# Optimization experiments

Measured on AMD Instinct MI355X. Metric: run time of the kernel, lower is better.

Reference implementation:

```python
import jax, jax.numpy as jnp
import numpy as np

N_QUBITS = 4
N_LAYERS = 2
BATCH = 524288


def _apply_1q(state, U, axis):
    # state: [B, 2,2,2,2]; U: [2,2] (shared) or [B,2,2] (per-sample); axis = wire index + 1
    s = jnp.moveaxis(state, axis, -1)
    if U.ndim == 3:
        s = jnp.einsum('bij,b...j->b...i', U, s)
    else:
        s = jnp.einsum('ij,...j->...i', U, s)
    return jnp.moveaxis(s, -1, axis)


def _apply_cz(state, a, b):
    # diagonal CZ: flip sign where both qubits are |1>
    sign = jnp.array([[1.0, 1.0], [1.0, -1.0]], dtype=state.dtype)
    shape = [1] * state.ndim
    shape[a] = 2
    shape[b] = 2
    return state * sign.reshape(shape)


def _quantum_expval(feats, w):
    # feats: [B, n_qubits] angles; w: [n_layers, n_qubits, 3] Rot params
    B = feats.shape[0]
    state = jnp.zeros((B,) + (2,) * N_QUBITS, jnp.complex64)
    state = state.at[(slice(None),) + (0,) * N_QUBITS].set(1.0)
    # per-sample RY embedding
    for i in range(N_QUBITS):
        c = jnp.cos(feats[:, i] * 0.5)
        s = jnp.sin(feats[:, i] * 0.5)
        U = jnp.stack([jnp.stack([c, -s], -1), jnp.stack([s, c], -1)], -2).astype(jnp.complex64)
        state = _apply_1q(state, U, i + 1)
    # variational layers: Rot(phi,theta,omega) = RZ(omega) RY(theta) RZ(phi), then CZ chain
    for l in range(N_LAYERS):
        for i in range(N_QUBITS):
            phi, theta, omega = w[l, i, 0], w[l, i, 1], w[l, i, 2]
            ct = jnp.cos(theta * 0.5)
            st = jnp.sin(theta * 0.5)
            U = jnp.stack([
                jnp.stack([jnp.exp(-0.5j * (phi + omega)) * ct, -jnp.exp(0.5j * (phi - omega)) * st]),
                jnp.stack([jnp.exp(-0.5j * (phi - omega)) * st, jnp.exp(0.5j * (phi + omega)) * ct]),
            ]).astype(jnp.complex64)
            state = _apply_1q(state, U, i + 1)
        for i in range(N_QUBITS - 1):
            state = _apply_cz(state, i + 1, i + 2)
    probs = jnp.square(jnp.abs(state))
    p = probs.sum(axis=tuple(range(2, N_QUBITS + 1)))  # marginal of wire 0 -> [B, 2]
    return (p[:, 0] - p[:, 1]).astype(jnp.float32)  # <Z_0>


def setup_inputs() -> dict:
    key = jax.random.key(0)
    ks = jax.random.split(key, 12)
    f = jnp.float32
    return {
        'text': jax.random.normal(ks[0], (BATCH, 16), f),
        'image': jax.random.normal(ks[1], (BATCH, 48), f),
        'tW1': jax.random.normal(ks[2], (16, 32), f) * 0.25,
        'tb1': jnp.zeros((32,), f),
        'tW2': jax.random.normal(ks[3], (32, N_QUBITS), f) * 0.18,
        'tb2': jnp.zeros((N_QUBITS,), f),
        'iW1': jax.random.normal(ks[4], (48, 64), f) * 0.14,
        'ib1': jnp.zeros((64,), f),
        'iW2': jax.random.normal(ks[5], (64, N_QUBITS), f) * 0.125,
        'ib2': jnp.zeros((N_QUBITS,), f),
        'qweights': jax.random.normal(ks[6], (N_LAYERS, N_QUBITS, 3), f),
        'cW1': jax.random.normal(ks[7], (1, 16), f),
        'cb1': jnp.zeros((16,), f),
        'cW2': jax.random.normal(ks[8], (16, 2), f) * 0.25,
        'cb2': jnp.zeros((2,), f),
    }


def reference(text, image, tW1, tb1, tW2, tb2, iW1, ib1, iW2, ib2, qweights, cW1, cb1, cW2, cb2):
    tf = jax.nn.relu(text @ tW1 + tb1) @ tW2 + tb2      # [B, 4]
    imf = jax.nn.relu(image @ iW1 + ib1) @ iW2 + ib2    # [B, 4]
    feats = (tf + imf) * 0.5                             # [B, 4]
    q = _quantum_expval(feats, qweights)                 # [B]
    h = jax.nn.relu(q[:, None] @ cW1 + cb1)              # [B, 16]
    return h @ cW2 + cb2                                 # [B, 2]
```

## Files before the change

### kernel.cpp

```cpp
#include <hip/hip_runtime.h>
#include <math.h>

#define NQ 4
#define NL 2

__global__ void qnn_precompute_A(const float* __restrict__ qw, float* __restrict__ A)
{
    __shared__ float Mre[16][16];
    __shared__ float Mim[16][16];
    int t = threadIdx.x;
    if (t < 16) {
        int j = t;
        float re[16], im[16];
        for (int b = 0; b < 16; ++b) { re[b] = (b == j) ? 1.f : 0.f; im[b] = 0.f; }
        for (int l = 0; l < NL; ++l) {
            for (int i = 0; i < NQ; ++i) {
                float phi   = qw[(l*NQ + i)*3 + 0];
                float theta = qw[(l*NQ + i)*3 + 1];
                float omega = qw[(l*NQ + i)*3 + 2];
                float ct, st; sincosf(0.5f*theta, &st, &ct);
                float ap = 0.5f*(phi + omega);
                float am = 0.5f*(phi - omega);
                float cap, sap, cam, sam;
                sincosf(ap, &sap, &cap);
                sincosf(am, &sam, &cam);
                float u00r =  cap*ct, u00i = -sap*ct;
                float u01r = -cam*st, u01i = -sam*st;
                float u10r =  cam*st, u10i = -sam*st;
                float u11r =  cap*ct, u11i =  sap*ct;
                int mask = 1 << (3 - i);
                for (int b = 0; b < 16; ++b) {
                    if (b & mask) continue;
                    int b1 = b | mask;
                    float a0r = re[b],  a0i = im[b];
                    float a1r = re[b1], a1i = im[b1];
                    re[b]  = u00r*a0r - u00i*a0i + u01r*a1r - u01i*a1i;
                    im[b]  = u00r*a0i + u00i*a0r + u01r*a1i + u01i*a1r;
                    re[b1] = u10r*a0r - u10i*a0i + u11r*a1r - u11i*a1i;
                    im[b1] = u10r*a0i + u10i*a0r + u11r*a1i + u11i*a1r;
                }
            }
            for (int b = 0; b < 16; ++b) {
                float sgn = 1.f;
                if ((b & 0xC) == 0xC) sgn = -sgn;
                if ((b & 0x6) == 0x6) sgn = -sgn;
                if ((b & 0x3) == 0x3) sgn = -sgn;
                re[b] *= sgn; im[b] *= sgn;
            }
        }
        for (int b = 0; b < 16; ++b) { Mre[j][b] = re[b]; Mim[j][b] = im[b]; }
    }
    __syncthreads();
    {
        int j = t >> 4, k = t & 15;
        float s = 0.f;
        #pragma unroll
        for (int b = 0; b < 16; ++b) {
            float sg = (b & 8) ? -1.f : 1.f;
            s += sg * (Mre[j][b]*Mre[k][b] + Mim[j][b]*Mim[k][b]);
        }
        A[j*16 + k] = s;
    }
}

__global__ __launch_bounds__(256, 4) void qnn_main(
    const float* __restrict__ text, const float* __restrict__ image,
    const float* __restrict__ tW1, const float* __restrict__ tb1,
    const float* __restrict__ tW2, const float* __restrict__ tb2,
    const float* __restrict__ iW1, const float* __restrict__ ib1,
    const float* __restrict__ iW2, const float* __restrict__ ib2,
    const float* __restrict__ A,
    const float* __restrict__ cW1, const float* __restrict__ cb1,
    const float* __restrict__ cW2, const float* __restrict__ cb2,
    float* __restrict__ out, int B)
{
    int b = blockIdx.x * blockDim.x + threadIdx.x;
    if (b >= B) return;

    float h2[64];
    #pragma unroll
    for (int j = 0; j < 64; ++j) h2[j] = ib1[j];
    {
        const float4* i4 = (const float4*)(image + (size_t)b * 48);
        #pragma unroll 2
        for (int k4 = 0; k4 < 12; ++k4) {
            float4 v = i4[k4];
            const float* w = iW1 + k4 * 4 * 64;
            #pragma unroll
            for (int j = 0; j < 64; ++j) h2[j] = fmaf(v.x, w[j],       h2[j]);
            #pragma unroll
            for (int j = 0; j < 64; ++j) h2[j] = fmaf(v.y, w[64 + j],  h2[j]);
            #pragma unroll
            for (int j = 0; j < 64; ++j) h2[j] = fmaf(v.z, w[128 + j], h2[j]);
            #pragma unroll
            for (int j = 0; j < 64; ++j) h2[j] = fmaf(v.w, w[192 + j], h2[j]);
        }
    }
    float imf[4];
    #pragma unroll
    for (int o = 0; o < 4; ++o) imf[o] = ib2[o];
    #pragma unroll
    for (int j = 0; j < 64; ++j) {
        float r = fmaxf(h2[j], 0.f);
        const float* w2 = iW2 + j * 4;
        #pragma unroll
        for (int o = 0; o < 4; ++o) imf[o] = fmaf(r, w2[o], imf[o]);
    }

    float h1[32];
    #pragma unroll
    for (int j = 0; j < 32; ++j) h1[j] = tb1[j];
    {
        const float4* t4 = (const float4*)(text + (size_t)b * 16);
        #pragma unroll
        for (int k4 = 0; k4 < 4; ++k4) {
            float4 v = t4[k4];
            const float* w = tW1 + k4 * 4 * 32;
            #pragma unroll
            for (int j = 0; j < 32; ++j) h1[j] = fmaf(v.x, w[j],      h1[j]);
            #pragma unroll
            for (int j = 0; j < 32; ++j) h1[j] = fmaf(v.y, w[32 + j], h1[j]);
            #pragma unroll
            for (int j = 0; j < 32; ++j) h1[j] = fmaf(v.z, w[64 + j], h1[j]);
            #pragma unroll
            for (int j = 0; j < 32; ++j) h1[j] = fmaf(v.w, w[96 + j], h1[j]);
        }
    }
    float tf[4];
    #pragma unroll
    for (int o = 0; o < 4; ++o) tf[o] = tb2[o];
    #pragma unroll
    for (int j = 0; j < 32; ++j) {
        float r = fmaxf(h1[j], 0.f);
        const float* w2 = tW2 + j * 4;
        #pragma unroll
        for (int o = 0; o < 4; ++o) tf[o] = fmaf(r, w2[o], tf[o]);
    }

    float c[4], s[4];
    #pragma unroll
    for (int i = 0; i < 4; ++i) {
        float f = (tf[i] + imf[i]) * 0.25f;
        __sincosf(f, &s[i], &c[i]);
    }
    float p01[4] = { c[0]*c[1], c[0]*s[1], s[0]*c[1], s[0]*s[1] };
    float p23[4] = { c[2]*c[3], c[2]*s[3], s[2]*c[3], s[2]*s[3] };
    float psi[16];
    #pragma unroll
    for (int x = 0; x < 4; ++x)
        #pragma unroll
        for (int y = 0; y < 4; ++y)
            psi[x*4+y] = p01[x] * p23[y];

    float q = 0.f;
    #pragma unroll
    for (int j = 0; j < 16; ++j) {
        float row = 0.f;
        #pragma unroll
        for (int k = 0; k < 16; ++k) row = fmaf(A[j*16+k], psi[k], row);
        q = fmaf(psi[j], row, q);
    }

    float o0 = cb2[0], o1 = cb2[1];
    #pragma unroll
    for (int j = 0; j < 16; ++j) {
        float h = fmaxf(fmaf(q, cW1[j], cb1[j]), 0.f);
        o0 = fmaf(h, cW2[j*2+0], o0);
        o1 = fmaf(h, cW2[j*2+1], o1);
    }
    float2* o2 = (float2*)out;
    o2[b] = make_float2(o0, o1);
}

extern "C" void kernel_launch(void* const* d_in, const int* in_sizes, int n_in,
                              void* d_out, int out_size, void* d_ws, size_t ws_size,
                              hipStream_t stream)
{
    const float* text  = (const float*)d_in[0];
    const float* image = (const float*)d_in[1];
    const float* tW1   = (const float*)d_in[2];
    const float* tb1   = (const float*)d_in[3];
    const float* tW2   = (const float*)d_in[4];
    const float* tb2   = (const float*)d_in[5];
    const float* iW1   = (const float*)d_in[6];
    const float* ib1   = (const float*)d_in[7];
    const float* iW2   = (const float*)d_in[8];
    const float* ib2   = (const float*)d_in[9];
    const float* qw    = (const float*)d_in[10];
    const float* cW1   = (const float*)d_in[11];
    const float* cb1   = (const float*)d_in[12];
    const float* cW2   = (const float*)d_in[13];
    const float* cb2   = (const float*)d_in[14];

    float* A = (float*)d_ws;
    int B = in_sizes[0] / 16;

    qnn_precompute_A<<<1, 256, 0, stream>>>(qw, A);

    int block = 256;
    int grid = (B + block - 1) / block;
    qnn_main<<<grid, block, 0, stream>>>(
        text, image, tW1, tb1, tW2, tb2, iW1, ib1, iW2, ib2,
        A, cW1, cb1, cW2, cb2, (float*)d_out, B);
}
```

Baseline: 257.6 us.

## Fuse observable precompute into main kernel and process two samples per thread

Removes the separate single-block kernel that builds the 16x16 observable matrix. Every block now recomputes that matrix into shared memory before its main work. Each thread handles two batch samples so every weight load is reused across both, with float4 weight loads, and launch bounds drop to 2 waves per SIMD. The costs are redundant per-block unitary computation, a higher register count from two 64-wide accumulators, lower occupancy, and fast __sincosf for the weight angles.

```diff
diff --git a/kernel.cpp b/kernel.cpp
--- a/kernel.cpp
+++ b/kernel.cpp
@@ -4,31 +4,40 @@
 #define NQ 4
 #define NL 2
 
-__global__ void qnn_precompute_A(const float* __restrict__ qw, float* __restrict__ A)
+__global__ __launch_bounds__(256, 2) void qnn_fused(
+    const float* __restrict__ text, const float* __restrict__ image,
+    const float* __restrict__ tW1, const float* __restrict__ tb1,
+    const float* __restrict__ tW2, const float* __restrict__ tb2,
+    const float* __restrict__ iW1, const float* __restrict__ ib1,
+    const float* __restrict__ iW2, const float* __restrict__ ib2,
+    const float* __restrict__ qw,
+    const float* __restrict__ cW1, const float* __restrict__ cb1,
+    const float* __restrict__ cW2, const float* __restrict__ cb2,
+    float* __restrict__ out, int B)
 {
-    __shared__ float Mre[16][16];
-    __shared__ float Mim[16][16];
-    int t = threadIdx.x;
-    if (t < 16) {
-        int j = t;
+    __shared__ float Mre[16][16], Mim[16][16], As[16][16];
+    const int tid = threadIdx.x;
+
+    if (tid < 16) {
+        const int j = tid;
         float re[16], im[16];
+        #pragma unroll
         for (int b = 0; b < 16; ++b) { re[b] = (b == j) ? 1.f : 0.f; im[b] = 0.f; }
         for (int l = 0; l < NL; ++l) {
             for (int i = 0; i < NQ; ++i) {
                 float phi   = qw[(l*NQ + i)*3 + 0];
                 float theta = qw[(l*NQ + i)*3 + 1];
                 float omega = qw[(l*NQ + i)*3 + 2];
-                float ct, st; sincosf(0.5f*theta, &st, &ct);
-                float ap = 0.5f*(phi + omega);
-                float am = 0.5f*(phi - omega);
+                float ct, st; __sincosf(0.5f*theta, &st, &ct);
                 float cap, sap, cam, sam;
-                sincosf(ap, &sap, &cap);
-                sincosf(am, &sam, &cam);
+                __sincosf(0.5f*(phi + omega), &sap, &cap);
+                __sincosf(0.5f*(phi - omega), &sam, &cam);
                 float u00r =  cap*ct, u00i = -sap*ct;
                 float u01r = -cam*st, u01i = -sam*st;
                 float u10r =  cam*st, u10i = -sam*st;
                 float u11r =  cap*ct, u11i =  sap*ct;
                 int mask = 1 << (3 - i);
+                #pragma unroll
                 for (int b = 0; b < 16; ++b) {
                     if (b & mask) continue;
                     int b1 = b | mask;
@@ -40,6 +49,7 @@
                     im[b1] = u10r*a0i + u10i*a0r + u11r*a1i + u11i*a1r;
                 }
             }
+            #pragma unroll
             for (int b = 0; b < 16; ++b) {
                 float sgn = 1.f;
                 if ((b & 0xC) == 0xC) sgn = -sgn;
@@ -48,128 +58,190 @@
                 re[b] *= sgn; im[b] *= sgn;
             }
         }
+        #pragma unroll
         for (int b = 0; b < 16; ++b) { Mre[j][b] = re[b]; Mim[j][b] = im[b]; }
     }
     __syncthreads();
     {
-        int j = t >> 4, k = t & 15;
-        float s = 0.f;
+        int j = tid >> 4, k = tid & 15;
+        float sacc = 0.f;
         #pragma unroll
         for (int b = 0; b < 16; ++b) {
             float sg = (b & 8) ? -1.f : 1.f;
-            s += sg * (Mre[j][b]*Mre[k][b] + Mim[j][b]*Mim[k][b]);
-        }
-        A[j*16 + k] = s;
-    }
-}
-
-__global__ __launch_bounds__(256, 4) void qnn_main(
-    const float* __restrict__ text, const float* __restrict__ image,
-    const float* __restrict__ tW1, const float* __restrict__ tb1,
-    const float* __restrict__ tW2, const float* __restrict__ tb2,
-    const float* __restrict__ iW1, const float* __restrict__ ib1,
-    const float* __restrict__ iW2, const float* __restrict__ ib2,
-    const float* __restrict__ A,
-    const float* __restrict__ cW1, const float* __restrict__ cb1,
-    const float* __restrict__ cW2, const float* __restrict__ cb2,
-    float* __restrict__ out, int B)
-{
-    int b = blockIdx.x * blockDim.x + threadIdx.x;
-    if (b >= B) return;
-
-    float h2[64];
-    #pragma unroll
-    for (int j = 0; j < 64; ++j) h2[j] = ib1[j];
-    {
-        const float4* i4 = (const float4*)(image + (size_t)b * 48);
+            sacc += sg * (Mre[j][b]*Mre[k][b] + Mim[j][b]*Mim[k][b]);
+        }
+        As[j][k] = sacc;
+    }
+    __syncthreads();
+
+    const int s0 = blockIdx.x * 512 + tid;
+    const int s1 = s0 + 256;
+    const int c0 = (s0 < B) ? s0 : (B - 1);
+    const int c1 = (s1 < B) ? s1 : (B - 1);
+
+    float a0[64], a1[64];
+    {
+        const float4* bb = (const float4*)ib1;
+        #pragma unroll
+        for (int j4 = 0; j4 < 16; ++j4) {
+            float4 bv = bb[j4];
+            a0[4*j4] = bv.x; a0[4*j4+1] = bv.y; a0[4*j4+2] = bv.z; a0[4*j4+3] = bv.w;
+            a1[4*j4] = bv.x; a1[4*j4+1] = bv.y; a1[4*j4+2] = bv.z; a1[4*j4+3] = bv.w;
+        }
+    }
+    {
+        const float4* i40 = (const float4*)(image + (size_t)c0 * 48);
+        const float4* i41 = (const float4*)(image + (size_t)c1 * 48);
         #pragma unroll 2
         for (int k4 = 0; k4 < 12; ++k4) {
-            float4 v = i4[k4];
-            const float* w = iW1 + k4 * 4 * 64;
-            #pragma unroll
-            for (int j = 0; j < 64; ++j) h2[j] = fmaf(v.x, w[j],       h2[j]);
-            #pragma unroll
-            for (int j = 0; j < 64; ++j) h2[j] = fmaf(v.y, w[64 + j],  h2[j]);
-            #pragma unroll
-            for (int j = 0; j < 64; ++j) h2[j] = fmaf(v.z, w[128 + j], h2[j]);
-            #pragma unroll
-            for (int j = 0; j < 64; ++j) h2[j] = fmaf(v.w, w[192 + j], h2[j]);
-        }
-    }
-    float imf[4];
-    #pragma unroll
-    for (int o = 0; o < 4; ++o) imf[o] = ib2[o];
-    #pragma unroll
-    for (int j = 0; j < 64; ++j) {
-        float r = fmaxf(h2[j], 0.f);
-        const float* w2 = iW2 + j * 4;
-        #pragma unroll
-        for (int o = 0; o < 4; ++o) imf[o] = fmaf(r, w2[o], imf[o]);
-    }
-
-    float h1[32];
-    #pragma unroll
-    for (int j = 0; j < 32; ++j) h1[j] = tb1[j];
-    {
-        const float4* t4 = (const float4*)(text + (size_t)b * 16);
+            float4 v0 = i40[k4];
+            float4 v1 = i41[k4];
+            const float4* wr = (const float4*)(iW1 + k4 * 4 * 64);
+            #pragma unroll
+            for (int kk = 0; kk < 4; ++kk) {
+                float e0 = (kk == 0) ? v0.x : (kk == 1) ? v0.y : (kk == 2) ? v0.z : v0.w;
+                float e1 = (kk == 0) ? v1.x : (kk == 1) ? v1.y : (kk == 2) ? v1.z : v1.w;
+                #pragma unroll
+                for (int j4 = 0; j4 < 16; ++j4) {
+                    float4 w = wr[kk*16 + j4];
+                    a0[4*j4]   = fmaf(e0, w.x, a0[4*j4]);
+                    a0[4*j4+1] = fmaf(e0, w.y, a0[4*j4+1]);
+                    a0[4*j4+2] = fmaf(e0, w.z, a0[4*j4+2]);
+                    a0[4*j4+3] = fmaf(e0, w.w, a0[4*j4+3]);
+                    a1[4*j4]   = fmaf(e1, w.x, a1[4*j4]);
+                    a1[4*j4+1] = fmaf(e1, w.y, a1[4*j4+1]);
+                    a1[4*j4+2] = fmaf(e1, w.z, a1[4*j4+2]);
+                    a1[4*j4+3] = fmaf(e1, w.w, a1[4*j4+3]);
+                }
+            }
+        }
+    }
+    float imf0[4], imf1[4];
+    {
+        float4 b2 = *(const float4*)ib2;
+        imf0[0] = b2.x; imf0[1] = b2.y; imf0[2] = b2.z; imf0[3] = b2.w;
+        imf1[0] = b2.x; imf1[1] = b2.y; imf1[2] = b2.z; imf1[3] = b2.w;
+        #pragma unroll 8
+        for (int j = 0; j < 64; ++j) {
+            float4 w2 = *(const float4*)(iW2 + j * 4);
+            float r0 = fmaxf(a0[j], 0.f);
+            float r1 = fmaxf(a1[j], 0.f);
+            imf0[0] = fmaf(r0, w2.x, imf0[0]); imf0[1] = fmaf(r0, w2.y, imf0[1]);
+            imf0[2] = fmaf(r0, w2.z, imf0[2]); imf0[3] = fmaf(r0, w2.w, imf0[3]);
+            imf1[0] = fmaf(r1, w2.x, imf1[0]); imf1[1] = fmaf(r1, w2.y, imf1[1]);
+            imf1[2] = fmaf(r1, w2.z, imf1[2]); imf1[3] = fmaf(r1, w2.w, imf1[3]);
+        }
+    }
+
+    {
+        const float4* bb = (const float4*)tb1;
+        #pragma unroll
+        for (int j4 = 0; j4 < 8; ++j4) {
+            float4 bv = bb[j4];
+            a0[4*j4] = bv.x; a0[4*j4+1] = bv.y; a0[4*j4+2] = bv.z; a0[4*j4+3] = bv.w;
+            a1[4*j4] = bv.x; a1[4*j4+1] = bv.y; a1[4*j4+2] = bv.z; a1[4*j4+3] = bv.w;
+        }
+        const float4* t40 = (const float4*)(text + (size_t)c0 * 16);
+        const float4* t41 = (const float4*)(text + (size_t)c1 * 16);
         #pragma unroll
         for (int k4 = 0; k4 < 4; ++k4) {
-            float4 v = t4[k4];
-            const float* w = tW1 + k4 * 4 * 32;
-            #pragma unroll
-            for (int j = 0; j < 32; ++j) h1[j] = fmaf(v.x, w[j],      h1[j]);
-            #pragma unroll
-            for (int j = 0; j < 32; ++j) h1[j] = fmaf(v.y, w[32 + j], h1[j]);
-            #pragma unroll
-            for (int j = 0; j < 32; ++j) h1[j] = fmaf(v.z, w[64 + j], h1[j]);
-            #pragma unroll
-            for (int j = 0; j < 32; ++j) h1[j] = fmaf(v.w, w[96 + j], h1[j]);
-        }
-    }
-    float tf[4];
-    #pragma unroll
-    for (int o = 0; o < 4; ++o) tf[o] = tb2[o];
-    #pragma unroll
-    for (int j = 0; j < 32; ++j) {
-        float r = fmaxf(h1[j], 0.f);
-        const float* w2 = tW2 + j * 4;
-        #pragma unroll
-        for (int o = 0; o < 4; ++o) tf[o] = fmaf(r, w2[o], tf[o]);
-    }
-
-    float c[4], s[4];
-    #pragma unroll
-    for (int i = 0; i < 4; ++i) {
-        float f = (tf[i] + imf[i]) * 0.25f;
-        __sincosf(f, &s[i], &c[i]);
-    }
-    float p01[4] = { c[0]*c[1], c[0]*s[1], s[0]*c[1], s[0]*s[1] };
-    float p23[4] = { c[2]*c[3], c[2]*s[3], s[2]*c[3], s[2]*s[3] };
-    float psi[16];
-    #pragma unroll
-    for (int x = 0; x < 4; ++x)
-        #pragma unroll
-        for (int y = 0; y < 4; ++y)
-            psi[x*4+y] = p01[x] * p23[y];
-
-    float q = 0.f;
+            float4 v0 = t40[k4];
+            float4 v1 = t41[k4];
+            const float4* wr = (const float4*)(tW1 + k4 * 4 * 32);
+            #pragma unroll
+            for (int kk = 0; kk < 4; ++kk) {
+                float e0 = (kk == 0) ? v0.x : (kk == 1) ? v0.y : (kk == 2) ? v0.z : v0.w;
+                float e1 = (kk == 0) ? v1.x : (kk == 1) ? v1.y : (kk == 2) ? v1.z : v1.w;
+                #pragma unroll
+                for (int j4 = 0; j4 < 8; ++j4) {
+                    float4 w = wr[kk*8 + j4];
+                    a0[4*j4]   = fmaf(e0, w.x, a0[4*j4]);
+                    a0[4*j4+1] = fmaf(e0, w.y, a0[4*j4+1]);
+                    a0[4*j4+2] = fmaf(e0, w.z, a0[4*j4+2]);
+                    a0[4*j4+3] = fmaf(e0, w.w, a0[4*j4+3]);
+                    a1[4*j4]   = fmaf(e1, w.x, a1[4*j4]);
+                    a1[4*j4+1] = fmaf(e1, w.y, a1[4*j4+1]);
+                    a1[4*j4+2] = fmaf(e1, w.z, a1[4*j4+2]);
+                    a1[4*j4+3] = fmaf(e1, w.w, a1[4*j4+3]);
+                }
+            }
+        }
+    }
+    float tf0[4], tf1[4];
+    {
+        float4 b2 = *(const float4*)tb2;
+        tf0[0] = b2.x; tf0[1] = b2.y; tf0[2] = b2.z; tf0[3] = b2.w;
+        tf1[0] = b2.x; tf1[1] = b2.y; tf1[2] = b2.z; tf1[3] = b2.w;
+        #pragma unroll 8
+        for (int j = 0; j < 32; ++j) {
+            float4 w2 = *(const float4*)(tW2 + j * 4);
+            float r0 = fmaxf(a0[j], 0.f);
+            float r1 = fmaxf(a1[j], 0.f);
+            tf0[0] = fmaf(r0, w2.x, tf0[0]); tf0[1] = fmaf(r0, w2.y, tf0[1]);
+            tf0[2] = fmaf(r0, w2.z, tf0[2]); tf0[3] = fmaf(r0, w2.w, tf0[3]);
+            tf1[0] = fmaf(r1, w2.x, tf1[0]); tf1[1] = fmaf(r1, w2.y, tf1[1]);
+            tf1[2] = fmaf(r1, w2.z, tf1[2]); tf1[3] = fmaf(r1, w2.w, tf1[3]);
+        }
+    }
+
+    float psi0[16], psi1[16];
+    {
+        float c[4], s[4];
+        #pragma unroll
+        for (int i = 0; i < 4; ++i) {
+            float f = (tf0[i] + imf0[i]) * 0.25f;
+            __sincosf(f, &s[i], &c[i]);
+        }
+        float p01[4] = { c[0]*c[1], c[0]*s[1], s[0]*c[1], s[0]*s[1] };
+        float p23[4] = { c[2]*c[3], c[2]*s[3], s[2]*c[3], s[2]*s[3] };
+        #pragma unroll
+        for (int x = 0; x < 4; ++x)
+            #pragma unroll
+            for (int y = 0; y < 4; ++y)
+                psi0[x*4+y] = p01[x] * p23[y];
+        #pragma unroll
+        for (int i = 0; i < 4; ++i) {
+            float f = (tf1[i] + imf1[i]) * 0.25f;
+            __sincosf(f, &s[i], &c[i]);
+        }
+        float q01[4] = { c[0]*c[1], c[0]*s[1], s[0]*c[1], s[0]*s[1] };
+        float q23[4] = { c[2]*c[3], c[2]*s[3], s[2]*c[3], s[2]*s[3] };
+        #pragma unroll
+        for (int x = 0; x < 4; ++x)
+            #pragma unroll
+            for (int y = 0; y < 4; ++y)
+                psi1[x*4+y] = q01[x] * q23[y];
+    }
+    float q0 = 0.f, q1 = 0.f;
     #pragma unroll
     for (int j = 0; j < 16; ++j) {
-        float row = 0.f;
-        #pragma unroll
-        for (int k = 0; k < 16; ++k) row = fmaf(A[j*16+k], psi[k], row);
-        q = fmaf(psi[j], row, q);
-    }
-
-    float o0 = cb2[0], o1 = cb2[1];
+        float r0 = 0.f, r1 = 0.f;
+        #pragma unroll
+        for (int k4 = 0; k4 < 4; ++k4) {
+            float4 av = *(const float4*)&As[j][k4*4];
+            r0 = fmaf(av.x, psi0[k4*4+0], r0); r0 = fmaf(av.y, psi0[k4*4+1], r0);
+            r0 = fmaf(av.z, psi0[k4*4+2], r0); r0 = fmaf(av.w, psi0[k4*4+3], r0);
+            r1 = fmaf(av.x, psi1[k4*4+0], r1); r1 = fmaf(av.y, psi1[k4*4+1], r1);
+            r1 = fmaf(av.z, psi1[k4*4+2], r1); r1 = fmaf(av.w, psi1[k4*4+3], r1);
+        }
+        q0 = fmaf(psi0[j], r0, q0);
+        q1 = fmaf(psi1[j], r1, q1);
+    }
+
+    float2 ob = *(const float2*)cb2;
+    float o00 = ob.x, o01 = ob.y, o10 = ob.x, o11 = ob.y;
     #pragma unroll
     for (int j = 0; j < 16; ++j) {
-        float h = fmaxf(fmaf(q, cW1[j], cb1[j]), 0.f);
-        o0 = fmaf(h, cW2[j*2+0], o0);
-        o1 = fmaf(h, cW2[j*2+1], o1);
+        float w1 = cW1[j], b1v = cb1[j];
+        float2 w2 = *(const float2*)(cW2 + j*2);
+        float h0 = fmaxf(fmaf(q0, w1, b1v), 0.f);
+        float h1 = fmaxf(fmaf(q1, w1, b1v), 0.f);
+        o00 = fmaf(h0, w2.x, o00); o01 = fmaf(h0, w2.y, o01);
+        o10 = fmaf(h1, w2.x, o10); o11 = fmaf(h1, w2.y, o11);
     }
     float2* o2 = (float2*)out;
-    o2[b] = make_float2(o0, o1);
+    if (s0 < B) o2[s0] = make_float2(o00, o01);
+    if (s1 < B) o2[s1] = make_float2(o10, o11);
 }
 
 extern "C" void kernel_launch(void* const* d_in, const int* in_sizes, int n_in,
@@ -192,14 +264,10 @@
     const float* cW2   = (const float*)d_in[13];
     const float* cb2   = (const float*)d_in[14];
 
-    float* A = (float*)d_ws;
     int B = in_sizes[0] / 16;
-
-    qnn_precompute_A<<<1, 256, 0, stream>>>(qw, A);
-
-    int block = 256;
-    int grid = (B + block - 1) / block;
-    qnn_main<<<grid, block, 0, stream>>>(
+    int grid = (B + 511) / 512;
+
+    qnn_fused<<<grid, 256, 0, stream>>>(
         text, image, tW1, tb1, tW2, tb2, iW1, ib1, iW2, ib2,
-        A, cW1, cb1, cW2, cb2, (float*)d_out, B);
+        qw, cW1, cb1, cW2, cb2, (float*)d_out, B);
 }
```

After: 1.019 ms. 3.96x slower.

## Fuse A precompute into main kernel and stage all weights in LDS

Applied to the files above, without the earlier changes.

Removes the separate single-block precompute launch. Every block now recomputes the 16x16 quantum observable matrix itself and copies all MLP weights into shared memory, so the inner loops read weights as LDS float4 instead of uniform global/scalar loads. This saves a kernel launch and the serial dependency between the two kernels. In exchange each of the 2048 blocks repeats the small circuit simulation on 16 threads and pays an LDS fill plus two barriers. The switch to fast __sincosf for the circuit angles may slightly change precision.

```diff
diff --git a/kernel.cpp b/kernel.cpp
--- a/kernel.cpp
+++ b/kernel.cpp
@@ -4,31 +4,67 @@
 #define NQ 4
 #define NL 2
 
-__global__ void qnn_precompute_A(const float* __restrict__ qw, float* __restrict__ A)
+#define O_IW1 0
+#define O_IW2 3072
+#define O_TW1 3328
+#define O_TW2 3840
+#define O_IB1 3968
+#define O_TB1 4032
+#define O_FB2 4064
+#define O_CW1 4068
+#define O_CB1 4084
+#define O_CW2 4100
+#define O_CB2 4132
+#define O_AS  4136
+#define O_MRE 4392
+#define O_MIM 4648
+#define LDS_FLOATS 4904
+
+__global__ __launch_bounds__(256, 4) void qnn_fused(
+    const float* __restrict__ text, const float* __restrict__ image,
+    const float* __restrict__ tW1, const float* __restrict__ tb1,
+    const float* __restrict__ tW2, const float* __restrict__ tb2,
+    const float* __restrict__ iW1, const float* __restrict__ ib1,
+    const float* __restrict__ iW2, const float* __restrict__ ib2,
+    const float* __restrict__ qw,
+    const float* __restrict__ cW1, const float* __restrict__ cb1,
+    const float* __restrict__ cW2, const float* __restrict__ cb2,
+    float* __restrict__ out, int B)
 {
-    __shared__ float Mre[16][16];
-    __shared__ float Mim[16][16];
-    int t = threadIdx.x;
-    if (t < 16) {
-        int j = t;
+    __shared__ __align__(16) float W[LDS_FLOATS];
+    const int tid = threadIdx.x;
+
+    for (int i = tid; i < 3072; i += 256) W[O_IW1 + i] = iW1[i];
+    W[O_IW2 + tid] = iW2[tid];
+    for (int i = tid; i < 512; i += 256) W[O_TW1 + i] = tW1[i];
+    if (tid < 128) W[O_TW2 + tid] = tW2[tid];
+    if (tid < 64)  W[O_IB1 + tid] = ib1[tid];
+    if (tid < 32)  W[O_TB1 + tid] = tb1[tid];
+    if (tid < 4)   W[O_FB2 + tid] = ib2[tid] + tb2[tid];
+    if (tid < 16) { W[O_CW1 + tid] = cW1[tid]; W[O_CB1 + tid] = cb1[tid]; }
+    if (tid < 32)  W[O_CW2 + tid] = cW2[tid];
+    if (tid < 2)   W[O_CB2 + tid] = cb2[tid];
+
+    if (tid < 16) {
+        const int j = tid;
         float re[16], im[16];
+        #pragma unroll
         for (int b = 0; b < 16; ++b) { re[b] = (b == j) ? 1.f : 0.f; im[b] = 0.f; }
         for (int l = 0; l < NL; ++l) {
             for (int i = 0; i < NQ; ++i) {
                 float phi   = qw[(l*NQ + i)*3 + 0];
                 float theta = qw[(l*NQ + i)*3 + 1];
                 float omega = qw[(l*NQ + i)*3 + 2];
-                float ct, st; sincosf(0.5f*theta, &st, &ct);
-                float ap = 0.5f*(phi + omega);
-                float am = 0.5f*(phi - omega);
+                float ct, st; __sincosf(0.5f*theta, &st, &ct);
                 float cap, sap, cam, sam;
-                sincosf(ap, &sap, &cap);
-                sincosf(am, &sam, &cam);
+                __sincosf(0.5f*(phi + omega), &sap, &cap);
+                __sincosf(0.5f*(phi - omega), &sam, &cam);
                 float u00r =  cap*ct, u00i = -sap*ct;
                 float u01r = -cam*st, u01i = -sam*st;
                 float u10r =  cam*st, u10i = -sam*st;
                 float u11r =  cap*ct, u11i =  sap*ct;
                 int mask = 1 << (3 - i);
+                #pragma unroll
                 for (int b = 0; b < 16; ++b) {
                     if (b & mask) continue;
                     int b1 = b | mask;
@@ -40,6 +76,7 @@
                     im[b1] = u10r*a0i + u10i*a0r + u11r*a1i + u11i*a1r;
                 }
             }
+            #pragma unroll
             for (int b = 0; b < 16; ++b) {
                 float sgn = 1.f;
                 if ((b & 0xC) == 0xC) sgn = -sgn;
@@ -48,103 +85,110 @@
                 re[b] *= sgn; im[b] *= sgn;
             }
         }
-        for (int b = 0; b < 16; ++b) { Mre[j][b] = re[b]; Mim[j][b] = im[b]; }
+        #pragma unroll
+        for (int b = 0; b < 16; ++b) { W[O_MRE + j*16 + b] = re[b]; W[O_MIM + j*16 + b] = im[b]; }
     }
     __syncthreads();
     {
-        int j = t >> 4, k = t & 15;
-        float s = 0.f;
+        int j = tid >> 4, k = tid & 15;
+        float sacc = 0.f;
         #pragma unroll
         for (int b = 0; b < 16; ++b) {
             float sg = (b & 8) ? -1.f : 1.f;
-            s += sg * (Mre[j][b]*Mre[k][b] + Mim[j][b]*Mim[k][b]);
-        }
-        A[j*16 + k] = s;
-    }
-}
-
-__global__ __launch_bounds__(256, 4) void qnn_main(
-    const float* __restrict__ text, const float* __restrict__ image,
-    const float* __restrict__ tW1, const float* __restrict__ tb1,
-    const float* __restrict__ tW2, const float* __restrict__ tb2,
-    const float* __restrict__ iW1, const float* __restrict__ ib1,
-    const float* __restrict__ iW2, const float* __restrict__ ib2,
-    const float* __restrict__ A,
-    const float* __restrict__ cW1, const float* __restrict__ cb1,
-    const float* __restrict__ cW2, const float* __restrict__ cb2,
-    float* __restrict__ out, int B)
-{
-    int b = blockIdx.x * blockDim.x + threadIdx.x;
-    if (b >= B) return;
-
-    float h2[64];
-    #pragma unroll
-    for (int j = 0; j < 64; ++j) h2[j] = ib1[j];
+            sacc += sg * (W[O_MRE + j*16 + b]*W[O_MRE + k*16 + b] +
+                          W[O_MIM + j*16 + b]*W[O_MIM + k*16 + b]);
+        }
+        W[O_AS + tid] = sacc;
+    }
+    __syncthreads();
+
+    const int s = blockIdx.x * 256 + tid;
+    const int cs = (s < B) ? s : (B - 1);
+
+    const float4* Wi1 = (const float4*)&W[O_IW1];
+    const float4* Wi2 = (const float4*)&W[O_IW2];
+    const float4* Wt1 = (const float4*)&W[O_TW1];
+    const float4* Wt2 = (const float4*)&W[O_TW2];
+    const float4* Bi1 = (const float4*)&W[O_IB1];
+    const float4* Bt1 = (const float4*)&W[O_TB1];
+    const float4* As4 = (const float4*)&W[O_AS];
+
+    float acc[64];
+    #pragma unroll
+    for (int j4 = 0; j4 < 16; ++j4) {
+        float4 bv = Bi1[j4];
+        acc[4*j4] = bv.x; acc[4*j4+1] = bv.y; acc[4*j4+2] = bv.z; acc[4*j4+3] = bv.w;
+    }
     {
-        const float4* i4 = (const float4*)(image + (size_t)b * 48);
+        const float4* xg = (const float4*)(image + (size_t)cs * 48);
         #pragma unroll 2
         for (int k4 = 0; k4 < 12; ++k4) {
-            float4 v = i4[k4];
-            const float* w = iW1 + k4 * 4 * 64;
+            float4 x = xg[k4];
             #pragma unroll
-            for (int j = 0; j < 64; ++j) h2[j] = fmaf(v.x, w[j],       h2[j]);
+            for (int kk = 0; kk < 4; ++kk) {
+                float e = (kk == 0) ? x.x : (kk == 1) ? x.y : (kk == 2) ? x.z : x.w;
+                const float4* wr = Wi1 + (k4*4 + kk)*16;
+                #pragma unroll
+                for (int j4 = 0; j4 < 16; ++j4) {
+                    float4 w = wr[j4];
+                    acc[4*j4+0] = fmaf(e, w.x, acc[4*j4+0]);
+                    acc[4*j4+1] = fmaf(e, w.y, acc[4*j4+1]);
+                    acc[4*j4+2] = fmaf(e, w.z, acc[4*j4+2]);
+                    acc[4*j4+3] = fmaf(e, w.w, acc[4*j4+3]);
+                }
+            }
+        }
+    }
+    float f0, f1, f2, f3;
+    f0 = W[O_FB2+0]; f1 = W[O_FB2+1]; f2 = W[O_FB2+2]; f3 = W[O_FB2+3];
+    #pragma unroll
+    for (int j = 0; j < 64; ++j) {
+        float r = fmaxf(acc[j], 0.f);
+        float4 w2 = Wi2[j];
+        f0 = fmaf(r, w2.x, f0); f1 = fmaf(r, w2.y, f1);
+        f2 = fmaf(r, w2.z, f2); f3 = fmaf(r, w2.w, f3);
+    }
+
+    #pragma unroll
+    for (int j4 = 0; j4 < 8; ++j4) {
+        float4 bv = Bt1[j4];
+        acc[4*j4] = bv.x; acc[4*j4+1] = bv.y; acc[4*j4+2] = bv.z; acc[4*j4+3] = bv.w;
+    }
+    {
+        const float4* xg = (const float4*)(text + (size_t)cs * 16);
+        #pragma unroll
+        for (int k4 = 0; k4 < 4; ++k4) {
+            float4 x = xg[k4];
             #pragma unroll
-            for (int j = 0; j < 64; ++j) h2[j] = fmaf(v.y, w[64 + j],  h2[j]);
-            #pragma unroll
-            for (int j = 0; j < 64; ++j) h2[j] = fmaf(v.z, w[128 + j], h2[j]);
-            #pragma unroll
-            for (int j = 0; j < 64; ++j) h2[j] = fmaf(v.w, w[192 + j], h2[j]);
-        }
-    }
-    float imf[4];
-    #pragma unroll
-    for (int o = 0; o < 4; ++o) imf[o] = ib2[o];
-    #pragma unroll
-    for (int j = 0; j < 64; ++j) {
-        float r = fmaxf(h2[j], 0.f);
-        const float* w2 = iW2 + j * 4;
-        #pragma unroll
-        for (int o = 0; o < 4; ++o) imf[o] = fmaf(r, w2[o], imf[o]);
-    }
-
-    float h1[32];
-    #pragma unroll
-    for (int j = 0; j < 32; ++j) h1[j] = tb1[j];
-    {
-        const float4* t4 = (const float4*)(text + (size_t)b * 16);
-        #pragma unroll
-        for (int k4 = 0; k4 < 4; ++k4) {
-            float4 v = t4[k4];
-            const float* w = tW1 + k4 * 4 * 32;
-            #pragma unroll
-            for (int j = 0; j < 32; ++j) h1[j] = fmaf(v.x, w[j],      h1[j]);
-            #pragma unroll
-            for (int j = 0; j < 32; ++j) h1[j] = fmaf(v.y, w[32 + j], h1[j]);
-            #pragma unroll
-            for (int j = 0; j < 32; ++j) h1[j] = fmaf(v.z, w[64 + j], h1[j]);
-            #pragma unroll
-            for (int j = 0; j < 32; ++j) h1[j] = fmaf(v.w, w[96 + j], h1[j]);
-        }
-    }
-    float tf[4];
-    #pragma unroll
-    for (int o = 0; o < 4; ++o) tf[o] = tb2[o];
+            for (int kk = 0; kk < 4; ++kk) {
+                float e = (kk == 0) ? x.x : (kk == 1) ? x.y : (kk == 2) ? x.z : x.w;
+                const float4* wr = Wt1 + (k4*4 + kk)*8;
+                #pragma unroll
+                for (int j4 = 0; j4 < 8; ++j4) {
+                    float4 w = wr[j4];
+                    acc[4*j4+0] = fmaf(e, w.x, acc[4*j4+0]);
+                    acc[4*j4+1] = fmaf(e, w.y, acc[4*j4+1]);
+                    acc[4*j4+2] = fmaf(e, w.z, acc[4*j4+2]);
+                    acc[4*j4+3] = fmaf(e, w.w, acc[4*j4+3]);
+                }
+            }
+        }
+    }
     #pragma unroll
     for (int j = 0; j < 32; ++j) {
-        float r = fmaxf(h1[j], 0.f);
-        const float* w2 = tW2 + j * 4;
-        #pragma unroll
-        for (int o = 0; o < 4; ++o) tf[o] = fmaf(r, w2[o], tf[o]);
-    }
-
-    float c[4], s[4];
-    #pragma unroll
-    for (int i = 0; i < 4; ++i) {
-        float f = (tf[i] + imf[i]) * 0.25f;
-        __sincosf(f, &s[i], &c[i]);
-    }
-    float p01[4] = { c[0]*c[1], c[0]*s[1], s[0]*c[1], s[0]*s[1] };
-    float p23[4] = { c[2]*c[3], c[2]*s[3], s[2]*c[3], s[2]*s[3] };
+        float r = fmaxf(acc[j], 0.f);
+        float4 w2 = Wt2[j];
+        f0 = fmaf(r, w2.x, f0); f1 = fmaf(r, w2.y, f1);
+        f2 = fmaf(r, w2.z, f2); f3 = fmaf(r, w2.w, f3);
+    }
+
+    float c0,s0v,c1,s1v,c2,s2v,c3,s3v;
+    __sincosf(f0 * 0.25f, &s0v, &c0);
+    __sincosf(f1 * 0.25f, &s1v, &c1);
+    __sincosf(f2 * 0.25f, &s2v, &c2);
+    __sincosf(f3 * 0.25f, &s3v, &c3);
+    float p01[4] = { c0*c1, c0*s1v, s0v*c1, s0v*s1v };
+    float p23[4] = { c2*c3, c2*s3v, s2v*c3, s2v*s3v };
     float psi[16];
     #pragma unroll
     for (int x = 0; x < 4; ++x)
@@ -157,19 +201,24 @@
     for (int j = 0; j < 16; ++j) {
         float row = 0.f;
         #pragma unroll
-        for (int k = 0; k < 16; ++k) row = fmaf(A[j*16+k], psi[k], row);
+        for (int k4 = 0; k4 < 4; ++k4) {
+            float4 a = As4[j*4 + k4];
+            row = fmaf(a.x, psi[k4*4+0], row);
+            row = fmaf(a.y, psi[k4*4+1], row);
+            row = fmaf(a.z, psi[k4*4+2], row);
+            row = fmaf(a.w, psi[k4*4+3], row);
+        }
         q = fmaf(psi[j], row, q);
     }
 
-    float o0 = cb2[0], o1 = cb2[1];
+    float o0 = W[O_CB2+0], o1 = W[O_CB2+1];
     #pragma unroll
     for (int j = 0; j < 16; ++j) {
-        float h = fmaxf(fmaf(q, cW1[j], cb1[j]), 0.f);
-        o0 = fmaf(h, cW2[j*2+0], o0);
-        o1 = fmaf(h, cW2[j*2+1], o1);
-    }
-    float2* o2 = (float2*)out;
-    o2[b] = make_float2(o0, o1);
+        float h = fmaxf(fmaf(q, W[O_CW1+j], W[O_CB1+j]), 0.f);
+        o0 = fmaf(h, W[O_CW2 + j*2 + 0], o0);
+        o1 = fmaf(h, W[O_CW2 + j*2 + 1], o1);
+    }
+    if (s < B) ((float2*)out)[s] = make_float2(o0, o1);
 }
 
 extern "C" void kernel_launch(void* const* d_in, const int* in_sizes, int n_in,
@@ -192,14 +241,10 @@
     const float* cW2   = (const float*)d_in[13];
     const float* cb2   = (const float*)d_in[14];
 
-    float* A = (float*)d_ws;
     int B = in_sizes[0] / 16;
-
-    qnn_precompute_A<<<1, 256, 0, stream>>>(qw, A);
-
-    int block = 256;
-    int grid = (B + block - 1) / block;
-    qnn_main<<<grid, block, 0, stream>>>(
+    int grid = (B + 255) / 256;
+
+    qnn_fused<<<grid, 256, 0, stream>>>(
         text, image, tW1, tb1, tW2, tb2, iW1, ib1, iW2, ib2,
-        A, cW1, cb1, cW2, cb2, (float*)d_out, B);
+        qw, cW1, cb1, cW2, cb2, (float*)d_out, B);
 }
```

Result: slower. 342.4 us (+32.9%).
